# Optimization experiments

Measured on AMD Instinct MI355X. Metric: run time of the kernel, lower is better.

## Reference

```python
import jax, jax.numpy as jnp
import numpy as np

RES = 14
N = RES * RES
NH = 8
KD = 32
D = 128   # attn_ratio * key_dim
DH = 1024 # D * NH
DIM = 384
B = 128
SCALE = KD ** -0.5


def _bias_idxs():
    pts = [(i, j) for i in range(RES) for j in range(RES)]
    offs, idxs = {}, []
    for p1 in pts:
        for p2 in pts:
            o = (abs(p1[0] - p2[0]), abs(p1[1] - p2[1]))
            offs.setdefault(o, len(offs))
            idxs.append(offs[o])
    return np.array(idxs, np.int32).reshape(N, N), len(offs)

BIAS_IDXS, NUM_OFF = _bias_idxs()  # (N, N), 196 distinct |offset| pairs


def setup_inputs() -> dict:
    key = jax.random.key(0)
    ks = jax.random.split(key, 32)
    g = lambda i, shape, s=0.05: jax.random.normal(ks[i], shape, jnp.float32) * s
    pos = lambda i, shape: jax.random.uniform(ks[i], shape, jnp.float32, minval=0.5, maxval=1.5)
    return dict(
        x=jax.random.normal(ks[0], (B, DIM, RES, RES), jnp.float32),
        qw=g(1, (NH * KD, DIM)), qb=g(2, (NH * KD,)), q_s=pos(3, (NH * KD,)), q_t=g(4, (NH * KD,)),
        kw=g(5, (NH * KD, DIM)), kb=g(6, (NH * KD,)), k_s=pos(7, (NH * KD,)), k_t=g(8, (NH * KD,)),
        vw=g(9, (DH, DIM)), vb=g(10, (DH,)), v_s=pos(11, (DH,)), v_t=g(12, (DH,)),
        lvw=g(13, (DH, 3, 3)), lvb=g(14, (DH,)), lv_s=pos(15, (DH,)), lv_t=g(16, (DH,)),
        th1w=g(17, (NH, NH), 0.3), th1b=g(18, (NH,)),
        th2w=g(19, (NH, NH), 0.3), th2b=g(20, (NH,)),
        ab=g(21, (NH, NUM_OFF)),
        pw=g(22, (DIM, DH)), pb=g(23, (DIM,)), p_s=pos(24, (DIM,)), p_t=g(25, (DIM,)),
    )


def _c(v):
    return v[None, :, None, None]


def conv1x1_bn(x, w, b, s, t):
    # 1x1 conv (NCHW) + eval-mode BN folded to per-channel affine
    y = jnp.einsum('bchw,oc->bohw', x, w) + _c(b)
    return y * _c(s) + _c(t)


def reference(x, qw, qb, q_s, q_t, kw, kb, k_s, k_t, vw, vb, v_s, v_t,
              lvw, lvb, lv_s, lv_t, th1w, th1b, th2w, th2b, ab,
              pw, pb, p_s, p_t):
    Bb = x.shape[0]
    # q,k: (B, NH, N, KD)
    q = conv1x1_bn(x, qw, qb, q_s, q_t).reshape(Bb, NH, KD, N).transpose(0, 1, 3, 2)
    k = conv1x1_bn(x, kw, kb, k_s, k_t).reshape(Bb, NH, KD, N).transpose(0, 1, 3, 2)
    v4 = conv1x1_bn(x, vw, vb, v_s, v_t)  # (B, DH, RES, RES)
    # local depthwise 3x3 conv + BN on v
    vl = jax.lax.conv_general_dilated(
        v4, lvw.reshape(DH, 1, 3, 3), window_strides=(1, 1), padding='SAME',
        dimension_numbers=('NCHW', 'OIHW', 'NCHW'), feature_group_count=DH)
    vl = (vl + _c(lvb)) * _c(lv_s) + _c(lv_t)
    v = v4.reshape(Bb, NH, D, N).transpose(0, 1, 3, 2)  # (B, NH, N, D)

    attn = jnp.einsum('bhid,bhjd->bhij', q, k) * SCALE
    attn = attn + ab[:, BIAS_IDXS][None]  # relative-position bias (1, NH, N, N)
    attn = jnp.einsum('bhij,gh->bgij', attn, th1w) + _c(th1b)  # talking head 1
    attn = jax.nn.softmax(attn, axis=-1)
    attn = jnp.einsum('bhij,gh->bgij', attn, th2w) + _c(th2b)  # talking head 2

    o = jnp.einsum('bhij,bhjd->bhid', attn, v)  # (B, NH, N, D)
    o = o.transpose(0, 1, 3, 2).reshape(Bb, DH, RES, RES) + vl
    o = jax.nn.relu(o)
    return conv1x1_bn(o, pw, pb, p_s, p_t)
```

## Files before the change

kernel.cpp:

```cpp
#include <hip/hip_runtime.h>
#include <hip/hip_bf16.h>
#include <stdint.h>

typedef __hip_bfloat16 bf16;
typedef short short8 __attribute__((ext_vector_type(8)));
typedef float f32x4 __attribute__((ext_vector_type(4)));

#define NB 128
#define NPIX 196
#define NPAD 208
#define VP 224
#define QROWS 208
#define NH 8
#define KD 32
#define DHEAD 128
#define DH 1024
#define DIM 384
#define NROWS (NB * NPAD)
#define SCALE 0.17677669529663687f

__device__ __forceinline__ float b2f(bf16 v) { return __bfloat162float(v); }
__device__ __forceinline__ bf16 f2b(float f) { return __float2bfloat16(f); }

__device__ __forceinline__ void gll16(const void* g, void* l) {
  auto gp = reinterpret_cast<const uint32_t __attribute__((address_space(1)))*>(
      reinterpret_cast<uintptr_t>(g));
  auto lp = reinterpret_cast<uint32_t __attribute__((address_space(3)))*>(
      reinterpret_cast<uintptr_t>(l));
  __builtin_amdgcn_global_load_lds(gp, lp, 16, 0, 0);
}

__global__ __launch_bounds__(256) void k_cvt(const float* __restrict__ src,
                                             bf16* __restrict__ dst, int n) {
  int i = blockIdx.x * 256 + threadIdx.x;
  if (i < n) dst[i] = f2b(src[i]);
}

__global__ __launch_bounds__(256) void k_xt(const float* __restrict__ x,
                                            bf16* __restrict__ XT) {
  __shared__ bf16 tile[32][33];
  int ct = blockIdx.x, nt = blockIdx.y, b = blockIdx.z;
  int c0 = ct * 32, n0 = nt * 32;
  int tc = threadIdx.x >> 5, tn = threadIdx.x & 31;
#pragma unroll
  for (int r = 0; r < 4; ++r) {
    int c = tc + r * 8;
    int n = n0 + tn;
    float v = 0.f;
    if (n < NPIX) v = x[((size_t)b * DIM + c0 + c) * NPIX + n];
    tile[c][tn] = f2b(v);
  }
  __syncthreads();
#pragma unroll
  for (int r = 0; r < 4; ++r) {
    int n = n0 + tc + r * 8;
    if (n < NPAD) XT[((size_t)b * NPAD + n) * DIM + c0 + tn] = tile[tn][tc + r * 8];
  }
}

__global__ __launch_bounds__(256, 2) void k_qkv2(
    const bf16* __restrict__ Wf, const bf16* __restrict__ XT,
    const float* __restrict__ qb, const float* __restrict__ qs, const float* __restrict__ qt,
    const float* __restrict__ kb, const float* __restrict__ ks, const float* __restrict__ kt,
    const float* __restrict__ vb, const float* __restrict__ vs, const float* __restrict__ vt,
    bf16* __restrict__ qf, bf16* __restrict__ kf, bf16* __restrict__ v4) {
  __shared__ __align__(16) char lds[2][32768];
  const int NWG = 12 * 208;
  int id = blockIdx.x;
  int id2 = (id & 7) * (NWG >> 3) + (id >> 3);
  int mt = id2 % 12, nt = id2 / 12;
  int m0 = mt * 128, n0 = nt * 128;
  int tid = threadIdx.x, lane = tid & 63;
  int wv = tid >> 6, wm = wv >> 1, wn = wv & 1;

  f32x4 acc[4][4];
#pragma unroll
  for (int mi = 0; mi < 4; ++mi)
#pragma unroll
    for (int ni = 0; ni < 4; ++ni)
#pragma unroll
      for (int r = 0; r < 4; ++r) acc[mi][ni][r] = 0.f;

  auto stage = [&](int buf, int t) {
    int k0 = t * 64;
#pragma unroll
    for (int j = 0; j < 4; ++j) {
      int gi = tid + j * 256;
      int row = gi >> 3, g = gi & 7;
      int sk = k0 + ((g ^ (row & 7)) << 3);
      gll16(Wf + (size_t)(m0 + row) * DIM + sk, &lds[buf][gi * 16]);
      gll16(XT + (size_t)(n0 + row) * DIM + sk, &lds[buf][16384 + gi * 16]);
    }
  };
  auto compute = [&](int buf) {
    const char* Ab = lds[buf];
    const char* Bb = lds[buf] + 16384;
    int kq = lane >> 4, il = lane & 15;
#pragma unroll
    for (int ksb = 0; ksb < 2; ++ksb) {
      int G = ksb * 4 + kq;
      short8 af[4], bfr[4];
#pragma unroll
      for (int mi = 0; mi < 4; ++mi) {
        int row = wm * 64 + mi * 16 + il;
        af[mi] = *(const short8*)(Ab + row * 128 + ((G ^ (row & 7)) << 4));
      }
#pragma unroll
      for (int ni = 0; ni < 4; ++ni) {
        int row = wn * 64 + ni * 16 + il;
        bfr[ni] = *(const short8*)(Bb + row * 128 + ((G ^ (row & 7)) << 4));
      }
#pragma unroll
      for (int mi = 0; mi < 4; ++mi)
#pragma unroll
        for (int ni = 0; ni < 4; ++ni)
          acc[mi][ni] = __builtin_amdgcn_mfma_f32_16x16x32_bf16(af[mi], bfr[ni], acc[mi][ni], 0, 0, 0);
    }
  };

  stage(0, 0);
  __syncthreads();
  for (int t = 0; t < 6; ++t) {
    if (t < 5) stage((t + 1) & 1, t + 1);
    compute(t & 1);
    __syncthreads();
  }

  int cq = lane >> 4, cn = lane & 15;
#pragma unroll
  for (int mi = 0; mi < 4; ++mi) {
    int mbase = m0 + wm * 64 + mi * 16;
    const float *bp, *sp, *tp;
    int segbase, segid;
    if (mbase < 256)      { bp = qb; sp = qs; tp = qt; segbase = 0;   segid = 0; }
    else if (mbase < 512) { bp = kb; sp = ks; tp = kt; segbase = 256; segid = 1; }
    else                  { bp = vb; sp = vs; tp = vt; segbase = 512; segid = 2; }
#pragma unroll
    for (int r = 0; r < 4; ++r) {
      int ms = mbase - segbase + cq * 4 + r;
      float bi = bp[ms], sc = sp[ms], tt = tp[ms];
#pragma unroll
      for (int ni = 0; ni < 4; ++ni) {
        int n = n0 + wn * 64 + ni * 16 + cn;
        int b = n / NPAD;
        int nn = n - b * NPAD;
        float y = (acc[mi][ni][r] + bi) * sc + tt;
        y = (nn < NPIX) ? y : 0.f;
        if (segid == 2) {
          v4[((size_t)b * DH + ms) * VP + nn] = f2b(y);
        } else {
          bf16* dst = segid ? kf : qf;
          dst[(((size_t)b * NH + (ms >> 5)) * QROWS + nn) * KD + (ms & 31)] = f2b(y);
        }
      }
    }
  }
}

__global__ __launch_bounds__(256) void k_vpad(bf16* __restrict__ v4) {
  int i = blockIdx.x * 256 + threadIdx.x;
  int tot = NB * DH * 16;
  if (i < tot) {
    int row = i >> 4, c = i & 15;
    v4[(size_t)row * VP + 208 + c] = f2b(0.f);
  }
}

__global__ __launch_bounds__(256, 2) void k_p2(
    const bf16* __restrict__ Pw, const bf16* __restrict__ OT,
    const float* __restrict__ pb, const float* __restrict__ ps, const float* __restrict__ pt,
    float* __restrict__ out) {
  __shared__ __align__(16) char lds[2][32768];
  const int NWG = 3 * 208;
  int id = blockIdx.x;
  int id2 = (id & 7) * (NWG >> 3) + (id >> 3);
  int mt = id2 % 3, nt = id2 / 3;
  int m0 = mt * 128, n0 = nt * 128;
  int tid = threadIdx.x, lane = tid & 63;
  int wv = tid >> 6, wm = wv >> 1, wn = wv & 1;

  f32x4 acc[4][4];
#pragma unroll
  for (int mi = 0; mi < 4; ++mi)
#pragma unroll
    for (int ni = 0; ni < 4; ++ni)
#pragma unroll
      for (int r = 0; r < 4; ++r) acc[mi][ni][r] = 0.f;

  auto stage = [&](int buf, int t) {
    int k0 = t * 64;
#pragma unroll
    for (int j = 0; j < 4; ++j) {
      int gi = tid + j * 256;
      int row = gi >> 3, g = gi & 7;
      int sk = k0 + ((g ^ (row & 7)) << 3);
      gll16(Pw + (size_t)(m0 + row) * DH + sk, &lds[buf][gi * 16]);
      gll16(OT + (size_t)(n0 + row) * DH + sk, &lds[buf][16384 + gi * 16]);
    }
  };
  auto compute = [&](int buf) {
    const char* Ab = lds[buf];
    const char* Bb = lds[buf] + 16384;
    int kq = lane >> 4, il = lane & 15;
#pragma unroll
    for (int ksb = 0; ksb < 2; ++ksb) {
      int G = ksb * 4 + kq;
      short8 af[4], bfr[4];
#pragma unroll
      for (int mi = 0; mi < 4; ++mi) {
        int row = wm * 64 + mi * 16 + il;
        af[mi] = *(const short8*)(Ab + row * 128 + ((G ^ (row & 7)) << 4));
      }
#pragma unroll
      for (int ni = 0; ni < 4; ++ni) {
        int row = wn * 64 + ni * 16 + il;
        bfr[ni] = *(const short8*)(Bb + row * 128 + ((G ^ (row & 7)) << 4));
      }
#pragma unroll
      for (int mi = 0; mi < 4; ++mi)
#pragma unroll
        for (int ni = 0; ni < 4; ++ni)
          acc[mi][ni] = __builtin_amdgcn_mfma_f32_16x16x32_bf16(af[mi], bfr[ni], acc[mi][ni], 0, 0, 0);
    }
  };

  stage(0, 0);
  __syncthreads();
  for (int t = 0; t < 16; ++t) {
    if (t < 15) stage((t + 1) & 1, t + 1);
    compute(t & 1);
    __syncthreads();
  }

  int cq = lane >> 4, cn = lane & 15;
#pragma unroll
  for (int mi = 0; mi < 4; ++mi) {
#pragma unroll
    for (int r = 0; r < 4; ++r) {
      int m = m0 + wm * 64 + mi * 16 + cq * 4 + r;
      float bi = pb[m], sc = ps[m], tt = pt[m];
#pragma unroll
      for (int ni = 0; ni < 4; ++ni) {
        int n = n0 + wn * 64 + ni * 16 + cn;
        int b = n / NPAD;
        int nn = n - b * NPAD;
        if (nn < NPIX)
          out[((size_t)b * DIM + m) * NPIX + nn] = (acc[mi][ni][r] + bi) * sc + tt;
      }
    }
  }
}

__global__ __launch_bounds__(256) void k_dw(
    const bf16* __restrict__ v4, const float* __restrict__ lvw,
    const float* __restrict__ lvb, const float* __restrict__ lvs,
    const float* __restrict__ lvt, bf16* __restrict__ vl) {
  int blk = blockIdx.x;
  int b = blk >> 8, cg = blk & 255;
  int lc = threadIdx.x >> 6, px = threadIdx.x & 63;
  int ch = cg * 4 + lc;
  const bf16* src = v4 + ((size_t)b * DH + ch) * VP;
  float w[9];
#pragma unroll
  for (int i = 0; i < 9; ++i) w[i] = lvw[ch * 9 + i];
  float bb = lvb[ch], ss = lvs[ch], tt = lvt[ch];
  bf16* dst = vl + ((size_t)b * DH + ch) * NPIX;
  for (int p = px; p < NPIX; p += 64) {
    int ri = p / 14, ci = p - ri * 14;
    float s = 0.f;
#pragma unroll
    for (int dy = -1; dy <= 1; ++dy)
#pragma unroll
      for (int dx = -1; dx <= 1; ++dx) {
        int rr = ri + dy, cc = ci + dx;
        if (rr >= 0 && rr < 14 && cc >= 0 && cc < 14)
          s += w[(dy + 1) * 3 + dx + 1] * b2f(src[rr * 14 + cc]);
      }
    dst[p] = f2b((s + bb) * ss + tt);
  }
}

__global__ __launch_bounds__(256) void k_vcs(const bf16* __restrict__ v4,
                                             float* __restrict__ vcs) {
  int b = blockIdx.x, g = blockIdx.y;
  int ch = g * 64 + (threadIdx.x >> 2);
  int part = threadIdx.x & 3;
  const bf16* src = v4 + ((size_t)b * DH + ch) * VP + part * 49;
  float s = 0.f;
  for (int j = 0; j < 49; ++j) s += b2f(src[j]);
  s += __shfl_xor(s, 1);
  s += __shfl_xor(s, 2);
  if (part == 0) vcs[b * DH + ch] = s;
}

#define SROW 448
__device__ __forceinline__ int saddr(int g, int i, int j) {
  int r = j * 2 + ((i & 7) << 4);
  if (r >= SROW) r -= SROW;
  return (g * 16 + i) * SROW + r;
}

__global__ __launch_bounds__(512, 2) void k_att(
    const bf16* __restrict__ qf, const bf16* __restrict__ kf,
    const bf16* __restrict__ v4, const bf16* __restrict__ vl,
    const float* __restrict__ vcs,
    const float* __restrict__ th1w, const float* __restrict__ th1b,
    const float* __restrict__ th2w, const float* __restrict__ th2b,
    const float* __restrict__ ab, bf16* __restrict__ OT) {
  __shared__ __align__(16) char smem[NH * 16 * SROW];
  __shared__ float ab2[NH * NPIX];
  __shared__ float c1[64];
  __shared__ float c2[64];
  int id = blockIdx.x;
  int xcd = id & 7;
  int rest = id >> 3;
  int qt = rest % 13;
  int b = (rest / 13) * 8 + xcd;
  int i0 = qt * 16;
  int tid = threadIdx.x;
  int wave = tid >> 6, lane = tid & 63;
  int il = lane & 15, kh = lane >> 4;

  if (tid < 64) {
    c1[tid] = th1w[tid] * SCALE;
    c2[tid] = th2w[tid];
  }
  for (int pos = tid; pos < NH * NPIX; pos += 512) {
    int g = pos / NPIX, off = pos - g * NPIX;
    float s = th1b[g];
#pragma unroll
    for (int h = 0; h < 8; ++h)
      s += th1w[g * 8 + h] * ab[h * NPIX + off];
    ab2[pos] = s;
  }
  {
    const bf16* qp = qf + ((size_t)b * NH + wave) * QROWS * KD;
    const bf16* kp = kf + ((size_t)b * NH + wave) * QROWS * KD;
    short8 a = *(const short8*)(qp + (i0 + il) * KD + kh * 8);
    for (int jt = 0; jt < 13; ++jt) {
      short8 bb = *(const short8*)(kp + (jt * 16 + il) * KD + kh * 8);
      f32x4 acc = {0.f, 0.f, 0.f, 0.f};
      acc = __builtin_amdgcn_mfma_f32_16x16x32_bf16(a, bb, acc, 0, 0, 0);
      int j = jt * 16 + il;
#pragma unroll
      for (int r = 0; r < 4; ++r)
        *(bf16*)(smem + saddr(wave, kh * 4 + r, j)) = f2b(acc[r]);
    }
  }
  __syncthreads();
  for (int pos = tid; pos < 16 * NPIX; pos += 512) {
    int i = pos / NPIX, j = pos - i * NPIX;
    float sv[8];
#pragma unroll
    for (int h = 0; h < 8; ++h) sv[h] = b2f(*(const bf16*)(smem + saddr(h, i, j)));
    int ia = i0 + i; if (ia > 195) ia = 195;
    int ri = ia / 14, ci = ia - ri * 14;
    int rj = j / 14, cj = j - rj * 14;
    int dr = ri > rj ? ri - rj : rj - ri;
    int dc = ci > cj ? ci - cj : cj - ci;
    int off = dr * 14 + dc;
    float outv[8];
#pragma unroll
    for (int g = 0; g < 8; ++g) {
      float s = ab2[g * NPIX + off];
#pragma unroll
      for (int h = 0; h < 8; ++h) s += c1[g * 8 + h] * sv[h];
      outv[g] = s;
    }
#pragma unroll
    for (int g = 0; g < 8; ++g)
      *(bf16*)(smem + saddr(g, i, j)) = f2b(outv[g]);
  }
  __syncthreads();
  {
    int row = tid >> 2, part = tid & 3;
    int g = row >> 4, i = row & 15;
    int jb = part * 49, je = jb + 49;
    float m = -1e30f;
    for (int j = jb; j < je; ++j)
      m = fmaxf(m, b2f(*(const bf16*)(smem + saddr(g, i, j))));
    m = fmaxf(m, __shfl_xor(m, 1));
    m = fmaxf(m, __shfl_xor(m, 2));
    float s = 0.f;
    for (int j = jb; j < je; ++j)
      s += __expf(b2f(*(const bf16*)(smem + saddr(g, i, j))) - m);
    s += __shfl_xor(s, 1);
    s += __shfl_xor(s, 2);
    float inv = 1.f / s;
    for (int j = jb; j < je; ++j) {
      bf16* p = (bf16*)(smem + saddr(g, i, j));
      *p = f2b(__expf(b2f(*p) - m) * inv);
    }
    if (part == 3)
      for (int j = NPIX; j < VP; ++j)
        *(bf16*)(smem + saddr(g, i, j)) = f2b(0.f);
  }
  __syncthreads();
  for (int pos = tid; pos < 16 * NPIX; pos += 512) {
    int i = pos / NPIX, j = pos - i * NPIX;
    float pv[8];
#pragma unroll
    for (int g = 0; g < 8; ++g) pv[g] = b2f(*(const bf16*)(smem + saddr(g, i, j)));
#pragma unroll
    for (int g2 = 0; g2 < 8; ++g2) {
      float s = 0.f;
#pragma unroll
      for (int g = 0; g < 8; ++g) s += c2[g2 * 8 + g] * pv[g];
      *(bf16*)(smem + saddr(g2, i, j)) = f2b(s);
    }
  }
  __syncthreads();
  {
    int g = wave;
    f32x4 oacc[8];
#pragma unroll
    for (int dt = 0; dt < 8; ++dt)
#pragma unroll
      for (int r = 0; r < 4; ++r) oacc[dt][r] = 0.f;
    const bf16* vbase = v4 + ((size_t)b * DH + g * DHEAD) * VP;
    for (int ks = 0; ks < 7; ++ks) {
      short8 pa = *(const short8*)(smem + saddr(g, il, ks * 32 + kh * 8));
#pragma unroll
      for (int dt = 0; dt < 8; ++dt) {
        short8 bv = *(const short8*)(vbase + (size_t)(dt * 16 + il) * VP + ks * 32 + kh * 8);
        oacc[dt] = __builtin_amdgcn_mfma_f32_16x16x32_bf16(pa, bv, oacc[dt], 0, 0, 0);
      }
    }
    float t2b = th2b[g];
#pragma unroll
    for (int dt = 0; dt < 8; ++dt) {
      int ch = g * DHEAD + dt * 16 + il;
      float csv = vcs[b * DH + ch] * t2b;
#pragma unroll
      for (int r = 0; r < 4; ++r) {
        int n = i0 + kh * 4 + r;
        if (n < NPIX) {
          float val = oacc[dt][r] + csv + b2f(vl[((size_t)b * DH + ch) * NPIX + n]);
          OT[((size_t)b * NPAD + n) * DH + ch] = f2b(fmaxf(val, 0.f));
        } else {
          OT[((size_t)b * NPAD + n) * DH + ch] = f2b(0.f);
        }
      }
    }
  }
}

extern "C" void kernel_launch(void* const* d_in, const int* in_sizes, int n_in,
                              void* d_out, int out_size, void* d_ws, size_t ws_size,
                              hipStream_t stream) {
  const float* x    = (const float*)d_in[0];
  const float* qw   = (const float*)d_in[1];
  const float* qb   = (const float*)d_in[2];
  const float* q_s  = (const float*)d_in[3];
  const float* q_t  = (const float*)d_in[4];
  const float* kw   = (const float*)d_in[5];
  const float* kb   = (const float*)d_in[6];
  const float* k_s  = (const float*)d_in[7];
  const float* k_t  = (const float*)d_in[8];
  const float* vw   = (const float*)d_in[9];
  const float* vb   = (const float*)d_in[10];
  const float* v_s  = (const float*)d_in[11];
  const float* v_t  = (const float*)d_in[12];
  const float* lvw  = (const float*)d_in[13];
  const float* lvb  = (const float*)d_in[14];
  const float* lv_s = (const float*)d_in[15];
  const float* lv_t = (const float*)d_in[16];
  const float* th1w = (const float*)d_in[17];
  const float* th1b = (const float*)d_in[18];
  const float* th2w = (const float*)d_in[19];
  const float* th2b = (const float*)d_in[20];
  const float* ab   = (const float*)d_in[21];
  const float* pw   = (const float*)d_in[22];
  const float* pb   = (const float*)d_in[23];
  const float* p_s  = (const float*)d_in[24];
  const float* p_t  = (const float*)d_in[25];

  char* ws = (char*)d_ws;
  size_t off = 0;
  auto alloc = [&](size_t bytes) {
    char* p = ws + off;
    off += (bytes + 255) & ~(size_t)255;
    return p;
  };
  char* region0 = alloc((size_t)NB * NPAD * DH * 2);
  bf16* XT  = (bf16*)region0;
  bf16* OT  = (bf16*)region0;
  bf16* qfb = (bf16*)alloc((size_t)NB * NH * QROWS * KD * 2);
  bf16* kfb = (bf16*)alloc((size_t)NB * NH * QROWS * KD * 2);
  bf16* v4  = (bf16*)alloc((size_t)NB * DH * VP * 2);
  bf16* vlb = (bf16*)alloc((size_t)NB * DH * NPIX * 2);
  float* vcs = (float*)alloc((size_t)NB * DH * 4);
  bf16* wf  = (bf16*)alloc((size_t)1536 * DIM * 2);
  bf16* wpb = (bf16*)alloc((size_t)DIM * DH * 2);
  (void)ws_size; (void)in_sizes; (void)n_in; (void)out_size;

  k_cvt<<<dim3((256 * DIM + 255) / 256), 256, 0, stream>>>(qw, wf, 256 * DIM);
  k_cvt<<<dim3((256 * DIM + 255) / 256), 256, 0, stream>>>(kw, wf + 256 * DIM, 256 * DIM);
  k_cvt<<<dim3((DH * DIM + 255) / 256), 256, 0, stream>>>(vw, wf + 512 * DIM, DH * DIM);
  k_cvt<<<dim3((DIM * DH + 255) / 256), 256, 0, stream>>>(pw, wpb, DIM * DH);
  k_xt<<<dim3(12, 7, NB), 256, 0, stream>>>(x, XT);
  k_qkv2<<<dim3(2496), 256, 0, stream>>>(wf, XT, qb, q_s, q_t, kb, k_s, k_t,
                                         vb, v_s, v_t, qfb, kfb, v4);
  k_vpad<<<dim3((NB * DH * 16 + 255) / 256), 256, 0, stream>>>(v4);
  k_dw<<<dim3(NB * 256), 256, 0, stream>>>(v4, lvw, lvb, lv_s, lv_t, vlb);
  k_vcs<<<dim3(NB, 16), 256, 0, stream>>>(v4, vcs);
  k_att<<<dim3(1664), 512, 0, stream>>>(qfb, kfb, v4, vlb, vcs,
                                        th1w, th1b, th2w, th2b, ab, OT);
  k_p2<<<dim3(624), 256, 0, stream>>>(wpb, OT, pb, p_s, p_t, (float*)d_out);
}
```

Measured before the change: 447.4 us.

## Vectorize attention LDS passes and fold softmax normalization into talking-head-2

The talking-head and softmax passes in the attention kernel now read and write score tiles in LDS as 4-element bf16 vectors instead of single elements, with the relative-bias offsets computed for four columns at a time. Softmax no longer makes a third normalisation pass: it stores unnormalised exponentials, saves per-row reciprocals in shared memory, and applies them inside the second talking-head mix. This cuts LDS traffic and per-element address arithmetic. The launch-bounds occupancy hint is also raised from 2 to 4 blocks per CU, which may force register spills.

```diff
diff --git a/kernel.cpp b/kernel.cpp
--- a/kernel.cpp
+++ b/kernel.cpp
@@ -3,6 +3,7 @@
 #include <stdint.h>
 
 typedef __hip_bfloat16 bf16;
+typedef short short4v __attribute__((ext_vector_type(4)));
 typedef short short8 __attribute__((ext_vector_type(8)));
 typedef float f32x4 __attribute__((ext_vector_type(4)));
 
@@ -16,11 +17,17 @@
 #define DHEAD 128
 #define DH 1024
 #define DIM 384
-#define NROWS (NB * NPAD)
 #define SCALE 0.17677669529663687f
 
 __device__ __forceinline__ float b2f(bf16 v) { return __bfloat162float(v); }
 __device__ __forceinline__ bf16 f2b(float f) { return __float2bfloat16(f); }
+__device__ __forceinline__ float us2f(unsigned short u) {
+  union { unsigned int i; float f; } v; v.i = (unsigned int)u << 16; return v.f;
+}
+__device__ __forceinline__ short f2us(float f) {
+  bf16 b = __float2bfloat16(f);
+  return *(short*)&b;
+}
 
 __device__ __forceinline__ void gll16(const void* g, void* l) {
   auto gp = reinterpret_cast<const uint32_t __attribute__((address_space(1)))*>(
@@ -300,7 +307,7 @@
   return (g * 16 + i) * SROW + r;
 }
 
-__global__ __launch_bounds__(512, 2) void k_att(
+__global__ __launch_bounds__(512, 4) void k_att(
     const bf16* __restrict__ qf, const bf16* __restrict__ kf,
     const bf16* __restrict__ v4, const bf16* __restrict__ vl,
     const float* __restrict__ vcs,
@@ -309,8 +316,9 @@
     const float* __restrict__ ab, bf16* __restrict__ OT) {
   __shared__ __align__(16) char smem[NH * 16 * SROW];
   __shared__ float ab2[NH * NPIX];
-  __shared__ float c1[64];
-  __shared__ float c2[64];
+  __shared__ float c1s[64];
+  __shared__ float c2s[64];
+  __shared__ float smInv[NH * 16];
   int id = blockIdx.x;
   int xcd = id & 7;
   int rest = id >> 3;
@@ -322,8 +330,8 @@
   int il = lane & 15, kh = lane >> 4;
 
   if (tid < 64) {
-    c1[tid] = th1w[tid] * SCALE;
-    c2[tid] = th2w[tid];
+    c1s[tid] = th1w[tid] * SCALE;
+    c2s[tid] = th2w[tid];
   }
   for (int pos = tid; pos < NH * NPIX; pos += 512) {
     int g = pos / NPIX, off = pos - g * NPIX;
@@ -348,65 +356,109 @@
     }
   }
   __syncthreads();
-  for (int pos = tid; pos < 16 * NPIX; pos += 512) {
-    int i = pos / NPIX, j = pos - i * NPIX;
-    float sv[8];
-#pragma unroll
-    for (int h = 0; h < 8; ++h) sv[h] = b2f(*(const bf16*)(smem + saddr(h, i, j)));
+  for (int item = tid; item < 16 * 52; item += 512) {
+    int i = item / 52, jq = item - i * 52;
+    int j0 = jq * 4;
+    float sv[8][4];
+#pragma unroll
+    for (int h = 0; h < 8; ++h) {
+      short4v v = *(const short4v*)(smem + saddr(h, i, j0));
+#pragma unroll
+      for (int t = 0; t < 4; ++t) sv[h][t] = us2f((unsigned short)v[t]);
+    }
     int ia = i0 + i; if (ia > 195) ia = 195;
     int ri = ia / 14, ci = ia - ri * 14;
-    int rj = j / 14, cj = j - rj * 14;
-    int dr = ri > rj ? ri - rj : rj - ri;
-    int dc = ci > cj ? ci - cj : cj - ci;
-    int off = dr * 14 + dc;
-    float outv[8];
+    int off4[4];
+    {
+      int rj = j0 / 14, cj = j0 - rj * 14;
+#pragma unroll
+      for (int t = 0; t < 4; ++t) {
+        if (cj >= 14) { cj -= 14; ++rj; }
+        int dr = ri > rj ? ri - rj : rj - ri;
+        int dc = ci > cj ? ci - cj : cj - ci;
+        off4[t] = (j0 + t < NPIX) ? dr * 14 + dc : 0;
+        ++cj;
+      }
+    }
 #pragma unroll
     for (int g = 0; g < 8; ++g) {
-      float s = ab2[g * NPIX + off];
-#pragma unroll
-      for (int h = 0; h < 8; ++h) s += c1[g * 8 + h] * sv[h];
-      outv[g] = s;
-    }
-#pragma unroll
-    for (int g = 0; g < 8; ++g)
-      *(bf16*)(smem + saddr(g, i, j)) = f2b(outv[g]);
+      float o[4];
+#pragma unroll
+      for (int t = 0; t < 4; ++t) o[t] = ab2[g * NPIX + off4[t]];
+#pragma unroll
+      for (int h = 0; h < 8; ++h) {
+        float c = c1s[g * 8 + h];
+#pragma unroll
+        for (int t = 0; t < 4; ++t) o[t] += c * sv[h][t];
+      }
+      short4v w;
+#pragma unroll
+      for (int t = 0; t < 4; ++t) w[t] = f2us(o[t]);
+      *(short4v*)(smem + saddr(g, i, j0)) = w;
+    }
   }
   __syncthreads();
   {
     int row = tid >> 2, part = tid & 3;
     int g = row >> 4, i = row & 15;
-    int jb = part * 49, je = jb + 49;
+    int jb = part * 52;
+    int n4 = (part == 3) ? 10 : 13;
     float m = -1e30f;
-    for (int j = jb; j < je; ++j)
-      m = fmaxf(m, b2f(*(const bf16*)(smem + saddr(g, i, j))));
+    for (int it = 0; it < n4; ++it) {
+      short4v v = *(const short4v*)(smem + saddr(g, i, jb + it * 4));
+#pragma unroll
+      for (int t = 0; t < 4; ++t) m = fmaxf(m, us2f((unsigned short)v[t]));
+    }
     m = fmaxf(m, __shfl_xor(m, 1));
     m = fmaxf(m, __shfl_xor(m, 2));
     float s = 0.f;
-    for (int j = jb; j < je; ++j)
-      s += __expf(b2f(*(const bf16*)(smem + saddr(g, i, j))) - m);
+    for (int it = 0; it < n4; ++it) {
+      char* p = smem + saddr(g, i, jb + it * 4);
+      short4v v = *(const short4v*)p;
+      short4v w;
+#pragma unroll
+      for (int t = 0; t < 4; ++t) {
+        float e = __expf(us2f((unsigned short)v[t]) - m);
+        s += e;
+        w[t] = f2us(e);
+      }
+      *(short4v*)p = w;
+    }
+    if (part == 3) {
+      short4v z = {0, 0, 0, 0};
+#pragma unroll
+      for (int it = 0; it < 7; ++it)
+        *(short4v*)(smem + saddr(g, i, 196 + it * 4)) = z;
+    }
     s += __shfl_xor(s, 1);
     s += __shfl_xor(s, 2);
-    float inv = 1.f / s;
-    for (int j = jb; j < je; ++j) {
-      bf16* p = (bf16*)(smem + saddr(g, i, j));
-      *p = f2b(__expf(b2f(*p) - m) * inv);
-    }
-    if (part == 3)
-      for (int j = NPIX; j < VP; ++j)
-        *(bf16*)(smem + saddr(g, i, j)) = f2b(0.f);
-  }
-  __syncthreads();
-  for (int pos = tid; pos < 16 * NPIX; pos += 512) {
-    int i = pos / NPIX, j = pos - i * NPIX;
-    float pv[8];
-#pragma unroll
-    for (int g = 0; g < 8; ++g) pv[g] = b2f(*(const bf16*)(smem + saddr(g, i, j)));
-#pragma unroll
-    for (int g2 = 0; g2 < 8; ++g2) {
-      float s = 0.f;
-#pragma unroll
-      for (int g = 0; g < 8; ++g) s += c2[g2 * 8 + g] * pv[g];
-      *(bf16*)(smem + saddr(g2, i, j)) = f2b(s);
+    if (part == 0) smInv[row] = 1.f / s;
+  }
+  __syncthreads();
+  for (int item = tid; item < 16 * 49; item += 512) {
+    int i = item / 49, jq = item - i * 49;
+    int j0 = jq * 4;
+    float pv[8][4];
+#pragma unroll
+    for (int h = 0; h < 8; ++h) {
+      float inv = smInv[h * 16 + i];
+      short4v v = *(const short4v*)(smem + saddr(h, i, j0));
+#pragma unroll
+      for (int t = 0; t < 4; ++t) pv[h][t] = us2f((unsigned short)v[t]) * inv;
+    }
+#pragma unroll
+    for (int g = 0; g < 8; ++g) {
+      float o[4] = {0.f, 0.f, 0.f, 0.f};
+#pragma unroll
+      for (int h = 0; h < 8; ++h) {
+        float c = c2s[g * 8 + h];
+#pragma unroll
+        for (int t = 0; t < 4; ++t) o[t] += c * pv[h][t];
+      }
+      short4v w;
+#pragma unroll
+      for (int t = 0; t < 4; ++t) w[t] = f2us(o[t]);
+      *(short4v*)(smem + saddr(g, i, j0)) = w;
     }
   }
   __syncthreads();
```

After: 592.0 us. 1.32x slower.

## Fold talking-head-1 into QK MFMA and fuse small kernels

Applied to the files above, without the earlier changes.

Each attention wave now computes one output head directly by scaling each input head's Q fragment by th1w*scale and accumulating the QK MFMAs over all eight heads. The positional bias is added as scores are written to shared memory, which removes the separate shared-memory pass that mixed heads. The change also merges the four weight-conversion launches into one and computes the V channel sums inside the depthwise-conv kernel, dropping the k_vcs launch. In exchange it does eight times more QK MFMA work and more K loads per wave, and rounds the scaled Q to bf16 before the dot product.

```diff
diff --git a/kernel.cpp b/kernel.cpp
--- a/kernel.cpp
+++ b/kernel.cpp
@@ -16,11 +16,17 @@
 #define DHEAD 128
 #define DH 1024
 #define DIM 384
-#define NROWS (NB * NPAD)
 #define SCALE 0.17677669529663687f
 
 __device__ __forceinline__ float b2f(bf16 v) { return __bfloat162float(v); }
 __device__ __forceinline__ bf16 f2b(float f) { return __float2bfloat16(f); }
+__device__ __forceinline__ float us2f(unsigned short u) {
+  union { unsigned int i; float f; } v; v.i = (unsigned int)u << 16; return v.f;
+}
+__device__ __forceinline__ short f2us(float f) {
+  bf16 b = __float2bfloat16(f);
+  return *(short*)&b;
+}
 
 __device__ __forceinline__ void gll16(const void* g, void* l) {
   auto gp = reinterpret_cast<const uint32_t __attribute__((address_space(1)))*>(
@@ -30,10 +36,19 @@
   __builtin_amdgcn_global_load_lds(gp, lp, 16, 0, 0);
 }
 
-__global__ __launch_bounds__(256) void k_cvt(const float* __restrict__ src,
-                                             bf16* __restrict__ dst, int n) {
+__global__ __launch_bounds__(256) void k_cvt4(const float* __restrict__ s0,
+                                              const float* __restrict__ s1,
+                                              const float* __restrict__ s2,
+                                              const float* __restrict__ s3,
+                                              bf16* __restrict__ dst) {
   int i = blockIdx.x * 256 + threadIdx.x;
-  if (i < n) dst[i] = f2b(src[i]);
+  if (i >= 983040) return;
+  const float* src; int o;
+  if (i < 98304)       { src = s0; o = i; }
+  else if (i < 196608) { src = s1; o = i - 98304; }
+  else if (i < 589824) { src = s2; o = i - 196608; }
+  else                 { src = s3; o = i - 589824; }
+  dst[i] = f2b(src[o]);
 }
 
 __global__ __launch_bounds__(256) void k_xt(const float* __restrict__ x,
@@ -251,10 +266,11 @@
   }
 }
 
-__global__ __launch_bounds__(256) void k_dw(
+__global__ __launch_bounds__(256) void k_dwv(
     const bf16* __restrict__ v4, const float* __restrict__ lvw,
     const float* __restrict__ lvb, const float* __restrict__ lvs,
-    const float* __restrict__ lvt, bf16* __restrict__ vl) {
+    const float* __restrict__ lvt, bf16* __restrict__ vl,
+    float* __restrict__ vcs) {
   int blk = blockIdx.x;
   int b = blk >> 8, cg = blk & 255;
   int lc = threadIdx.x >> 6, px = threadIdx.x & 63;
@@ -265,6 +281,7 @@
   for (int i = 0; i < 9; ++i) w[i] = lvw[ch * 9 + i];
   float bb = lvb[ch], ss = lvs[ch], tt = lvt[ch];
   bf16* dst = vl + ((size_t)b * DH + ch) * NPIX;
+  float csum = 0.f;
   for (int p = px; p < NPIX; p += 64) {
     int ri = p / 14, ci = p - ri * 14;
     float s = 0.f;
@@ -276,21 +293,16 @@
         if (rr >= 0 && rr < 14 && cc >= 0 && cc < 14)
           s += w[(dy + 1) * 3 + dx + 1] * b2f(src[rr * 14 + cc]);
       }
+    csum += b2f(src[p]);
     dst[p] = f2b((s + bb) * ss + tt);
   }
-}
-
-__global__ __launch_bounds__(256) void k_vcs(const bf16* __restrict__ v4,
-                                             float* __restrict__ vcs) {
-  int b = blockIdx.x, g = blockIdx.y;
-  int ch = g * 64 + (threadIdx.x >> 2);
-  int part = threadIdx.x & 3;
-  const bf16* src = v4 + ((size_t)b * DH + ch) * VP + part * 49;
-  float s = 0.f;
-  for (int j = 0; j < 49; ++j) s += b2f(src[j]);
-  s += __shfl_xor(s, 1);
-  s += __shfl_xor(s, 2);
-  if (part == 0) vcs[b * DH + ch] = s;
+  csum += __shfl_xor(csum, 1);
+  csum += __shfl_xor(csum, 2);
+  csum += __shfl_xor(csum, 4);
+  csum += __shfl_xor(csum, 8);
+  csum += __shfl_xor(csum, 16);
+  csum += __shfl_xor(csum, 32);
+  if (px == 0) vcs[b * DH + ch] = csum;
 }
 
 #define SROW 448
@@ -309,8 +321,7 @@
     const float* __restrict__ ab, bf16* __restrict__ OT) {
   __shared__ __align__(16) char smem[NH * 16 * SROW];
   __shared__ float ab2[NH * NPIX];
-  __shared__ float c1[64];
-  __shared__ float c2[64];
+  __shared__ float c2s[64];
   int id = blockIdx.x;
   int xcd = id & 7;
   int rest = id >> 3;
@@ -321,10 +332,7 @@
   int wave = tid >> 6, lane = tid & 63;
   int il = lane & 15, kh = lane >> 4;
 
-  if (tid < 64) {
-    c1[tid] = th1w[tid] * SCALE;
-    c2[tid] = th2w[tid];
-  }
+  if (tid < 64) c2s[tid] = th2w[tid];
   for (int pos = tid; pos < NH * NPIX; pos += 512) {
     int g = pos / NPIX, off = pos - g * NPIX;
     float s = th1b[g];
@@ -333,43 +341,49 @@
       s += th1w[g * 8 + h] * ab[h * NPIX + off];
     ab2[pos] = s;
   }
+  __syncthreads();
   {
-    const bf16* qp = qf + ((size_t)b * NH + wave) * QROWS * KD;
-    const bf16* kp = kf + ((size_t)b * NH + wave) * QROWS * KD;
-    short8 a = *(const short8*)(qp + (i0 + il) * KD + kh * 8);
+    const bf16* qpb = qf + (size_t)b * NH * QROWS * KD + (size_t)(i0 + il) * KD + kh * 8;
+    const bf16* kpb = kf + (size_t)b * NH * QROWS * KD + (size_t)il * KD + kh * 8;
+    short8 qfr[8];
+#pragma unroll
+    for (int h = 0; h < 8; ++h) {
+      short8 raw = *(const short8*)(qpb + (size_t)h * QROWS * KD);
+      float c = th1w[wave * 8 + h] * SCALE;
+      short8 s;
+#pragma unroll
+      for (int e = 0; e < 8; ++e) s[e] = f2us(us2f((unsigned short)raw[e]) * c);
+      qfr[h] = s;
+    }
+    int ri4[4], ci4[4];
+#pragma unroll
+    for (int r = 0; r < 4; ++r) {
+      int ia = i0 + kh * 4 + r; if (ia > 195) ia = 195;
+      int rr = (ia * 4682) >> 16;
+      ri4[r] = rr; ci4[r] = ia - rr * 14;
+    }
     for (int jt = 0; jt < 13; ++jt) {
-      short8 bb = *(const short8*)(kp + (jt * 16 + il) * KD + kh * 8);
-      f32x4 acc = {0.f, 0.f, 0.f, 0.f};
-      acc = __builtin_amdgcn_mfma_f32_16x16x32_bf16(a, bb, acc, 0, 0, 0);
+      f32x4 a0 = {0.f, 0.f, 0.f, 0.f};
+      f32x4 a1 = {0.f, 0.f, 0.f, 0.f};
+#pragma unroll
+      for (int h = 0; h < 8; h += 2) {
+        short8 b0 = *(const short8*)(kpb + (size_t)h * QROWS * KD + jt * 16 * KD);
+        short8 b1 = *(const short8*)(kpb + (size_t)(h + 1) * QROWS * KD + jt * 16 * KD);
+        a0 = __builtin_amdgcn_mfma_f32_16x16x32_bf16(qfr[h], b0, a0, 0, 0, 0);
+        a1 = __builtin_amdgcn_mfma_f32_16x16x32_bf16(qfr[h + 1], b1, a1, 0, 0, 0);
+      }
       int j = jt * 16 + il;
-#pragma unroll
-      for (int r = 0; r < 4; ++r)
-        *(bf16*)(smem + saddr(wave, kh * 4 + r, j)) = f2b(acc[r]);
-    }
-  }
-  __syncthreads();
-  for (int pos = tid; pos < 16 * NPIX; pos += 512) {
-    int i = pos / NPIX, j = pos - i * NPIX;
-    float sv[8];
-#pragma unroll
-    for (int h = 0; h < 8; ++h) sv[h] = b2f(*(const bf16*)(smem + saddr(h, i, j)));
-    int ia = i0 + i; if (ia > 195) ia = 195;
-    int ri = ia / 14, ci = ia - ri * 14;
-    int rj = j / 14, cj = j - rj * 14;
-    int dr = ri > rj ? ri - rj : rj - ri;
-    int dc = ci > cj ? ci - cj : cj - ci;
-    int off = dr * 14 + dc;
-    float outv[8];
-#pragma unroll
-    for (int g = 0; g < 8; ++g) {
-      float s = ab2[g * NPIX + off];
-#pragma unroll
-      for (int h = 0; h < 8; ++h) s += c1[g * 8 + h] * sv[h];
-      outv[g] = s;
-    }
-#pragma unroll
-    for (int g = 0; g < 8; ++g)
-      *(bf16*)(smem + saddr(g, i, j)) = f2b(outv[g]);
+      int rj = (j * 4682) >> 16;
+      int cj = j - rj * 14;
+#pragma unroll
+      for (int r = 0; r < 4; ++r) {
+        int dr = ri4[r] > rj ? ri4[r] - rj : rj - ri4[r];
+        int dc = ci4[r] > cj ? ci4[r] - cj : cj - ci4[r];
+        int off = (j < NPIX) ? dr * 14 + dc : 0;
+        float v = a0[r] + a1[r] + ab2[wave * NPIX + off];
+        *(bf16*)(smem + saddr(wave, kh * 4 + r, j)) = f2b(v);
+      }
+    }
   }
   __syncthreads();
   {
@@ -405,7 +419,7 @@
     for (int g2 = 0; g2 < 8; ++g2) {
       float s = 0.f;
 #pragma unroll
-      for (int g = 0; g < 8; ++g) s += c2[g2 * 8 + g] * pv[g];
+      for (int g = 0; g < 8; ++g) s += c2s[g2 * 8 + g] * pv[g];
       *(bf16*)(smem + saddr(g2, i, j)) = f2b(s);
     }
   }
@@ -494,16 +508,12 @@
   bf16* wpb = (bf16*)alloc((size_t)DIM * DH * 2);
   (void)ws_size; (void)in_sizes; (void)n_in; (void)out_size;
 
-  k_cvt<<<dim3((256 * DIM + 255) / 256), 256, 0, stream>>>(qw, wf, 256 * DIM);
-  k_cvt<<<dim3((256 * DIM + 255) / 256), 256, 0, stream>>>(kw, wf + 256 * DIM, 256 * DIM);
-  k_cvt<<<dim3((DH * DIM + 255) / 256), 256, 0, stream>>>(vw, wf + 512 * DIM, DH * DIM);
-  k_cvt<<<dim3((DIM * DH + 255) / 256), 256, 0, stream>>>(pw, wpb, DIM * DH);
+  k_cvt4<<<dim3(3840), 256, 0, stream>>>(qw, kw, vw, pw, wf);
   k_xt<<<dim3(12, 7, NB), 256, 0, stream>>>(x, XT);
   k_qkv2<<<dim3(2496), 256, 0, stream>>>(wf, XT, qb, q_s, q_t, kb, k_s, k_t,
                                          vb, v_s, v_t, qfb, kfb, v4);
   k_vpad<<<dim3((NB * DH * 16 + 255) / 256), 256, 0, stream>>>(v4);
-  k_dw<<<dim3(NB * 256), 256, 0, stream>>>(v4, lvw, lvb, lv_s, lv_t, vlb);
-  k_vcs<<<dim3(NB, 16), 256, 0, stream>>>(v4, vcs);
+  k_dwv<<<dim3(NB * 256), 256, 0, stream>>>(v4, lvw, lvb, lv_s, lv_t, vlb, vcs);
   k_att<<<dim3(1664), 512, 0, stream>>>(qfb, kfb, v4, vlb, vcs,
                                         th1w, th1b, th2w, th2b, ab, OT);
   k_p2<<<dim3(624), 256, 0, stream>>>(wpb, OT, pb, p_s, p_t, (float*)d_out);
```

Measured after the change: 493.3 us. 1.1x slower.
